# Optimization experiments

Measured on AMD Instinct MI355X. Metric: run time of the kernel, lower is better.

Reference implementation:

```python
import jax, jax.numpy as jnp
import numpy as np

B, CIN, H, W = 64, 1, 64, 64
L = 6            # layer_number -> 2^L = 64 blocks per axis
T = 4            # chebyshev_number
C4 = 4 * T * T   # per-block channel width = 64
WK = H // 2 ** (L - 1)  # first-layer kernel/stride = 2
LEFT = H // 2 ** L      # leftover_x = leftover_y = 1


def setup_inputs() -> dict:
    key = jax.random.key(0)
    ks = jax.random.split(key, 16)
    d = {}
    d["x_real"] = jax.random.normal(ks[0], (B, CIN, H, W), jnp.float32)
    d["x_imag"] = jax.random.normal(ks[1], (B, CIN, H, W), jnp.float32)
    # layer 0: per-input-channel conv, 4 -> 4*C4 channels, kernel=stride=WK
    d["w0"] = jax.random.normal(ks[2], (CIN, 4 * C4, 4, WK, WK), jnp.float32) / float(np.sqrt(4 * WK * WK))
    d["b0"] = jnp.zeros((CIN, 4 * C4), jnp.float32)
    # recursion layers lyr=1..L-1: one conv per (channel, block), C4 -> 4*C4, kernel 2x2 stride 2
    for lyr in range(1, L):
        G = 2 ** lyr
        d["w%d" % lyr] = jax.random.normal(ks[2 + lyr], (CIN, G, G, 4 * C4, C4, 2, 2), jnp.float32) / float(np.sqrt(4 * C4))
        d["b%d" % lyr] = jnp.zeros((CIN, G, G, 4 * C4), jnp.float32)
    # final layer: 1x1 conv per block, C4 -> 4*LEFT*LEFT
    GL = 2 ** L
    d["wf"] = jax.random.normal(ks[10], (CIN, GL, GL, 4 * LEFT * LEFT, C4), jnp.float32) / float(np.sqrt(C4))
    d["bf"] = jnp.zeros((CIN, GL, GL, 4 * LEFT * LEFT), jnp.float32)
    return d


def _forward(x_real, x_imag, w0, b0, wrec, brec, wf, bf):
    # split(): [relu(re), relu(im), relu(-re), relu(-im)] per input channel
    xs = jax.nn.relu(jnp.stack([x_real, x_imag, -x_real, -x_imag], axis=2))  # (B,CIN,4,H,W)
    # layer 0: kernel=stride=WK conv as blocked einsum -> (B,CIN,4*C4,P,P), P = 2^(L-1)
    P = H // WK
    xb = xs.reshape(B, CIN, 4, P, WK, P, WK)
    y = jnp.einsum('bcipkql,coikl->bcopq', xb, w0) + b0[None, :, :, None, None]
    y = jax.nn.relu(y)
    # output channels = 2x2 block grid x C4; layout (B,CIN,gy,gx,C4,S,S)
    G, S = 2, P
    y = y.reshape(B, CIN, G, G, C4, S, S)
    for lyr in range(1, L):
        w, b = wrec[lyr - 1], brec[lyr - 1]
        S2 = S // 2
        # 2x2/stride-2 conv per block as batched einsum
        yb = y.reshape(B, CIN, G, G, C4, S2, 2, S2, 2)
        z = jnp.einsum('bcghipkql,cghoikl->bcghopq', yb, w) + b[None, :, :, :, :, None, None]
        z = jax.nn.relu(z)
        # out channels split into (y_loc,x_loc,C4); child block = (2*gy+y_loc, 2*gx+x_loc)
        z = z.reshape(B, CIN, G, G, 2, 2, C4, S2, S2)
        z = z.transpose(0, 1, 2, 4, 3, 5, 6, 7, 8).reshape(B, CIN, 2 * G, 2 * G, C4, S2, S2)
        y, G, S = z, 2 * G, S2
    # final layer: spatial S == 1, 1x1 conv per block
    yv = y[..., 0, 0]                                     # (B,CIN,GL,GL,C4)
    f = jnp.einsum('bcghi,cghoi->bcgho', yv, wf) + bf[None]
    f = jax.nn.relu(f)
    # out channel o = 4*(ky*LEFT+kx)+comp; pixel = (gy*LEFT+ky, gx*LEFT+kx)
    f = f.reshape(B, CIN, G, G, LEFT, LEFT, 4)
    f = f.transpose(0, 1, 2, 4, 3, 5, 6).reshape(B, CIN, H, W, 4)
    # joint(): real = comp0 - comp2, then scale by 1/(H*W)
    return (f[..., 0] - f[..., 2]) / (H * W)


def reference(x_real, x_imag, w0, b0, w1, b1, w2, b2, w3, b3, w4, b4, w5, b5, wf, bf):
    return _forward(x_real, x_imag, w0, b0, (w1, w2, w3, w4, w5), (b1, b2, b3, b4, b5), wf, bf)
```

## Files before the change

kernel.cpp:

```cpp
#include <hip/hip_runtime.h>
#include <cstddef>


typedef unsigned int  u32;
typedef unsigned short u16;
typedef __attribute__((ext_vector_type(8))) short bf16x8;
typedef __attribute__((ext_vector_type(4))) float f32x4;

#define PLANE 16777216

__device__ inline u16 bf16_rn(float x) {
    u32 u = __builtin_bit_cast(u32, x);
    u32 r = (u + 0x7FFFu + ((u >> 16) & 1u)) >> 16;
    return (u16)r;
}
__device__ inline float bf16_to_f(u16 h) {
    u32 u = ((u32)h) << 16;
    return __builtin_bit_cast(float, u);
}
__device__ inline u32 pack_split(float v) {
    const u16 h = bf16_rn(v);
    const u16 l = bf16_rn(v - bf16_to_f(h));
    return (u32)h | ((u32)l << 16);
}
__device__ inline void bar_lds() {
    asm volatile("s_waitcnt lgkmcnt(0)\n\ts_barrier" ::: "memory");
}

__global__ __launch_bounds__(256)
void wconv_kernel(const float* __restrict__ src, u16* __restrict__ hi,
                  u16* __restrict__ lo, int n8) {
    const int i = blockIdx.x * 256 + threadIdx.x;
    if (i >= n8) return;
    const float4 a = *(const float4*)(src + 8 * i);
    const float4 b = *(const float4*)(src + 8 * i + 4);
    union { bf16x8 v; u16 u[8]; } H, L;
    const float f[8] = {a.x, a.y, a.z, a.w, b.x, b.y, b.z, b.w};
#pragma unroll
    for (int e = 0; e < 8; ++e) {
        const u16 h = bf16_rn(f[e]);
        H.u[e] = h;
        L.u[e] = bf16_rn(f[e] - bf16_to_f(h));
    }
    *(bf16x8*)(hi + 8 * i) = H.v;
    *(bf16x8*)(lo + 8 * i) = L.v;
}

__global__ __launch_bounds__(256)
void layer0_kernel(const float* __restrict__ xr, const float* __restrict__ xi,
                   const float* __restrict__ w0, const float* __restrict__ b0,
                   u32* __restrict__ A1) {
    __shared__ float w0s[128][16];
    __shared__ float b0s[128];
    const int og  = blockIdx.y;
    const int tid = threadIdx.x;
    {
        const int row = tid >> 1, half = tid & 1;
        const float4 wa = *(const float4*)(w0 + (og * 128 + row) * 16 + half * 8);
        const float4 wb = *(const float4*)(w0 + (og * 128 + row) * 16 + half * 8 + 4);
        *(float4*)&w0s[row][half * 8]     = wa;
        *(float4*)&w0s[row][half * 8 + 4] = wb;
        if (tid < 128) b0s[tid] = b0[og * 128 + tid];
    }
    __syncthreads();

    const int n = blockIdx.x * 256 + tid;
    const int b = n >> 10, p = (n >> 5) & 31, q = n & 31;
    float xs[16];
#pragma unroll
    for (int k = 0; k < 2; ++k) {
        const float2 vr = *(const float2*)(xr + b * 4096 + (2 * p + k) * 64 + 2 * q);
        const float2 vi = *(const float2*)(xi + b * 4096 + (2 * p + k) * 64 + 2 * q);
        xs[0  + k * 2 + 0] = fmaxf(vr.x, 0.f);  xs[0  + k * 2 + 1] = fmaxf(vr.y, 0.f);
        xs[4  + k * 2 + 0] = fmaxf(vi.x, 0.f);  xs[4  + k * 2 + 1] = fmaxf(vi.y, 0.f);
        xs[8  + k * 2 + 0] = fmaxf(-vr.x, 0.f); xs[8  + k * 2 + 1] = fmaxf(-vr.y, 0.f);
        xs[12 + k * 2 + 0] = fmaxf(-vi.x, 0.f); xs[12 + k * 2 + 1] = fmaxf(-vi.y, 0.f);
    }
    const int kp = p & 1, lp = q & 1, pp = p >> 1, qp = q >> 1;
    const size_t pixoff = (size_t)(b * 256 + pp * 16 + qp);
#pragma unroll
    for (int j = 0; j < 128; ++j) {
        float acc = b0s[j];
#pragma unroll
        for (int e = 0; e < 16; ++e) acc = fmaf(xs[e], w0s[j][e], acc);
        acc = fmaxf(acc, 0.f);
        const int o = og * 128 + j;
        const int gy = o >> 7, gx = (o >> 6) & 1, c = o & 63;
        const size_t flat = (size_t)((((gy * 2 + gx) * 64 + c) * 2 + kp) * 2 + lp) * (64 * 256)
                          + pixoff;
        A1[flat] = pack_split(acc);
    }
}

template<int NT, bool PRECONV>
__global__ __launch_bounds__(256, 2)
void rec_mfma_kernel(const u32* __restrict__ Yg,
                     const float* __restrict__ Wf,
                     const u16* __restrict__ Whi_g, const u16* __restrict__ Wlo_g,
                     const float* __restrict__ bias, u32* __restrict__ Aout,
                     const int lgG, const int lgS2) {
    constexpr int NF  = NT / 16;
    constexpr int LD  = 40;
    constexpr int NCP = NT / 2;
    constexpr int NRG = 256 / NCP;
    constexpr int RPT = 32 / NRG;

    __shared__ u16 Yhi_s[NT * LD];
    __shared__ u16 Ylo_s[NT * LD];

    const int G  = 1 << lgG;
    const int S2 = 1 << lgS2;
    const int Nb = 64 << (2 * lgS2);

    int bid, nt;
    const int nBid = G * G, NTILES = gridDim.x;
    if (nBid >= 8) {
        const int h = blockIdx.z * NTILES + blockIdx.x;
        const int xcd = h & 7, j = h >> 3, per = nBid >> 3;
        bid = xcd * per + j / NTILES;
        nt  = j % NTILES;
    } else { bid = blockIdx.z; nt = blockIdx.x; }

    const size_t wbase = (size_t)bid * 65536;
    const u32* Yblk = Yg + (size_t)bid * 256 * (size_t)Nb + (size_t)nt * NT;

    const int tid = threadIdx.x, wave = tid >> 6, lane = tid & 63;
    const int l16 = lane & 15, lk = lane >> 4;
    const int cp = tid % NCP, rg = tid / NCP;
    const int col0 = cp * 2, trow = rg * RPT;

    f32x4 acc[4][NF];
#pragma unroll
    for (int m = 0; m < 4; ++m)
#pragma unroll
        for (int n = 0; n < NF; ++n)
            acc[m][n] = (f32x4){0.f, 0.f, 0.f, 0.f};

    uint2  yreg[2][RPT];
    float4 wv[2][8];
    bf16x8 wh[4], wl[4];
    u32 yhw[2][RPT / 2], ylw[2][RPT / 2];

    auto loadY = [&](int ybuf, int k0) {
#pragma unroll
        for (int r = 0; r < RPT; ++r)
            yreg[ybuf][r] = *(const uint2*)(Yblk + (size_t)(k0 + trow + r) * Nb + col0);
    };
    auto loadWpre = [&](int k0) {
#pragma unroll
        for (int m = 0; m < 4; ++m) {
            const size_t off = wbase + (size_t)(wave * 64 + m * 16 + l16) * 256 + k0 + lk * 8;
            wh[m] = *(const bf16x8*)(Whi_g + off);
            wl[m] = *(const bf16x8*)(Wlo_g + off);
        }
    };
    auto loadWf32 = [&](int wbuf, int k0) {
#pragma unroll
        for (int m = 0; m < 4; ++m) {
            const float* wr = Wf + wbase + (size_t)(wave * 64 + m * 16 + l16) * 256 + k0 + lk * 8;
            wv[wbuf][2 * m]     = *(const float4*)wr;
            wv[wbuf][2 * m + 1] = *(const float4*)(wr + 4);
        }
    };
    auto convW = [&](int wbuf) {
#pragma unroll
        for (int m = 0; m < 4; ++m) {
            const float f[8] = { wv[wbuf][2 * m].x,     wv[wbuf][2 * m].y,
                                 wv[wbuf][2 * m].z,     wv[wbuf][2 * m].w,
                                 wv[wbuf][2 * m + 1].x, wv[wbuf][2 * m + 1].y,
                                 wv[wbuf][2 * m + 1].z, wv[wbuf][2 * m + 1].w };
            union { bf16x8 v; u16 u[8]; } H, L;
#pragma unroll
            for (int e = 0; e < 8; ++e) {
                const u16 hh = bf16_rn(f[e]);
                H.u[e] = hh;
                L.u[e] = bf16_rn(f[e] - bf16_to_f(hh));
            }
            wh[m] = H.v;
            wl[m] = L.v;
        }
    };
    auto prepY = [&](int ybuf) {
#pragma unroll
        for (int c = 0; c < 2; ++c)
#pragma unroll
            for (int j2 = 0; j2 < RPT / 2; ++j2) {
                const u32 a = c ? yreg[ybuf][2 * j2].y     : yreg[ybuf][2 * j2].x;
                const u32 b = c ? yreg[ybuf][2 * j2 + 1].y : yreg[ybuf][2 * j2 + 1].x;
                yhw[c][j2] = (a & 0xFFFFu) | (b << 16);
                ylw[c][j2] = (a >> 16)     | (b & 0xFFFF0000u);
            }
    };
    auto stageY = [&]() {
#pragma unroll
        for (int c = 0; c < 2; ++c) {
            if constexpr (RPT == 8) {
                *(uint4*)&Yhi_s[(col0 + c) * LD + trow] = make_uint4(yhw[c][0], yhw[c][1], yhw[c][2], yhw[c][3]);
                *(uint4*)&Ylo_s[(col0 + c) * LD + trow] = make_uint4(ylw[c][0], ylw[c][1], ylw[c][2], ylw[c][3]);
            } else {
                *(uint2*)&Yhi_s[(col0 + c) * LD + trow] = make_uint2(yhw[c][0], yhw[c][1]);
                *(uint2*)&Ylo_s[(col0 + c) * LD + trow] = make_uint2(ylw[c][0], ylw[c][1]);
            }
        }
    };

    if constexpr (PRECONV) { loadY(0, 0); loadY(1, 32); }
    else { loadWf32(0, 0); loadY(0, 0); loadWf32(1, 32); loadY(1, 32); }

#pragma unroll
    for (int it = 0; it < 8; ++it) {
        const int k0 = it * 32;
        const int cur = it & 1;
        if constexpr (PRECONV) loadWpre(k0);
        else convW(cur);
        prepY(cur);
        bar_lds();
        stageY();
        bar_lds();
        if constexpr (PRECONV) {
            if (it + 2 < 8) loadY(cur, k0 + 64);
        } else {
            if (it + 2 < 8) { loadWf32(cur, k0 + 64); loadY(cur, k0 + 64); }
        }
        __builtin_amdgcn_s_setprio(1);
#pragma unroll
        for (int n = 0; n < NF; ++n) {
            const int ccol = n * 16 + l16;
            const bf16x8 bhi = *(const bf16x8*)&Yhi_s[ccol * LD + 8 * lk];
            const bf16x8 blo = *(const bf16x8*)&Ylo_s[ccol * LD + 8 * lk];
#pragma unroll
            for (int m = 0; m < 4; ++m)
                acc[m][n] = __builtin_amdgcn_mfma_f32_16x16x32_bf16(wh[m], bhi, acc[m][n], 0, 0, 0);
#pragma unroll
            for (int m = 0; m < 4; ++m)
                acc[m][n] = __builtin_amdgcn_mfma_f32_16x16x32_bf16(wh[m], blo, acc[m][n], 0, 0, 0);
#pragma unroll
            for (int m = 0; m < 4; ++m)
                acc[m][n] = __builtin_amdgcn_mfma_f32_16x16x32_bf16(wl[m], bhi, acc[m][n], 0, 0, 0);
        }
        __builtin_amdgcn_s_setprio(0);
    }

    const int gy = bid >> lgG, gx = bid & (G - 1);
    const int NS2 = S2 >> 1;
#pragma unroll
    for (int m = 0; m < 4; ++m) {
#pragma unroll
        for (int r = 0; r < 4; ++r) {
            const int oc = wave * 64 + m * 16 + lk * 4 + r;
            const float bi = bias[(size_t)bid * 256 + oc];
            const int yl = oc >> 7, xl = (oc >> 6) & 1, cch = oc & 63;
            const int cy = 2 * gy + yl, cx = 2 * gx + xl;
            const size_t base = (size_t)((cy * (2 * G) + cx) * 64 + cch);
#pragma unroll
            for (int n = 0; n < NF; ++n) {
                const float v = fmaxf(acc[m][n][r] + bi, 0.f);
                const int ng = nt * NT + n * 16 + l16;
                const int b   = ng >> (2 * lgS2);
                const int rem = ng & ((1 << (2 * lgS2)) - 1);
                const int p = rem >> lgS2, q = rem & (S2 - 1);
                const size_t flat = ((base * 2 + (p & 1)) * 2 + (q & 1)) * (size_t)(64 * NS2 * NS2)
                                  + (size_t)(b * NS2 * NS2 + (p >> 1) * NS2 + (q >> 1));
                Aout[flat] = pack_split(v);
            }
        }
    }
}

__global__ __launch_bounds__(256, 2)
void rec5_final_kernel(const u32* __restrict__ Yg, const float* __restrict__ Wf,
                       const float* __restrict__ bias, const float* __restrict__ wf,
                       const float* __restrict__ bff, float* __restrict__ out) {
    constexpr int NF = 4, LD = 40, RPT = 4;

    __shared__ u16 Yhi_s[64 * LD];
    __shared__ u16 Ylo_s[64 * LD];

    const int bid = blockIdx.x;
    const size_t wbase = (size_t)bid * 65536;
    const u32* Yblk = Yg + (size_t)bid * 256 * 64;

    const int tid = threadIdx.x, wave = tid >> 6, lane = tid & 63;
    const int l16 = lane & 15, lk = lane >> 4;
    const int cp = tid & 31, rg = tid >> 5;
    const int col0 = cp * 2, trow = rg * RPT;

    f32x4 acc[4][NF];
#pragma unroll
    for (int m = 0; m < 4; ++m)
#pragma unroll
        for (int n = 0; n < NF; ++n)
            acc[m][n] = (f32x4){0.f, 0.f, 0.f, 0.f};

    uint2  yreg[2][RPT];
    float4 wv[2][8];
    bf16x8 wh[4], wl[4];
    u32 yhw[2][RPT / 2], ylw[2][RPT / 2];

    auto loadY = [&](int ybuf, int k0) {
#pragma unroll
        for (int r = 0; r < RPT; ++r)
            yreg[ybuf][r] = *(const uint2*)(Yblk + (size_t)(k0 + trow + r) * 64 + col0);
    };
    auto loadWf32 = [&](int wbuf, int k0) {
#pragma unroll
        for (int m = 0; m < 4; ++m) {
            const float* wr = Wf + wbase + (size_t)(wave * 64 + m * 16 + l16) * 256 + k0 + lk * 8;
            wv[wbuf][2 * m]     = *(const float4*)wr;
            wv[wbuf][2 * m + 1] = *(const float4*)(wr + 4);
        }
    };
    auto convW = [&](int wbuf) {
#pragma unroll
        for (int m = 0; m < 4; ++m) {
            const float f[8] = { wv[wbuf][2 * m].x,     wv[wbuf][2 * m].y,
                                 wv[wbuf][2 * m].z,     wv[wbuf][2 * m].w,
                                 wv[wbuf][2 * m + 1].x, wv[wbuf][2 * m + 1].y,
                                 wv[wbuf][2 * m + 1].z, wv[wbuf][2 * m + 1].w };
            union { bf16x8 v; u16 u[8]; } H, L;
#pragma unroll
            for (int e = 0; e < 8; ++e) {
                const u16 hh = bf16_rn(f[e]);
                H.u[e] = hh;
                L.u[e] = bf16_rn(f[e] - bf16_to_f(hh));
            }
            wh[m] = H.v;
            wl[m] = L.v;
        }
    };

    loadWf32(0, 0); loadY(0, 0); loadWf32(1, 32); loadY(1, 32);

#pragma unroll
    for (int it = 0; it < 8; ++it) {
        const int k0 = it * 32;
        const int cur = it & 1;
        convW(cur);
#pragma unroll
        for (int c = 0; c < 2; ++c)
#pragma unroll
            for (int j2 = 0; j2 < RPT / 2; ++j2) {
                const u32 a = c ? yreg[cur][2 * j2].y     : yreg[cur][2 * j2].x;
                const u32 b = c ? yreg[cur][2 * j2 + 1].y : yreg[cur][2 * j2 + 1].x;
                yhw[c][j2] = (a & 0xFFFFu) | (b << 16);
                ylw[c][j2] = (a >> 16)     | (b & 0xFFFF0000u);
            }
        bar_lds();
#pragma unroll
        for (int c = 0; c < 2; ++c) {
            *(uint2*)&Yhi_s[(col0 + c) * LD + trow] = make_uint2(yhw[c][0], yhw[c][1]);
            *(uint2*)&Ylo_s[(col0 + c) * LD + trow] = make_uint2(ylw[c][0], ylw[c][1]);
        }
        bar_lds();
        if (it + 2 < 8) { loadWf32(cur, k0 + 64); loadY(cur, k0 + 64); }
        __builtin_amdgcn_s_setprio(1);
#pragma unroll
        for (int n = 0; n < NF; ++n) {
            const int ccol = n * 16 + l16;
            const bf16x8 bhi = *(const bf16x8*)&Yhi_s[ccol * LD + 8 * lk];
            const bf16x8 blo = *(const bf16x8*)&Ylo_s[ccol * LD + 8 * lk];
#pragma unroll
            for (int m = 0; m < 4; ++m)
                acc[m][n] = __builtin_amdgcn_mfma_f32_16x16x32_bf16(wh[m], bhi, acc[m][n], 0, 0, 0);
#pragma unroll
            for (int m = 0; m < 4; ++m)
                acc[m][n] = __builtin_amdgcn_mfma_f32_16x16x32_bf16(wh[m], blo, acc[m][n], 0, 0, 0);
#pragma unroll
            for (int m = 0; m < 4; ++m)
                acc[m][n] = __builtin_amdgcn_mfma_f32_16x16x32_bf16(wl[m], bhi, acc[m][n], 0, 0, 0);
        }
        __builtin_amdgcn_s_setprio(0);
    }

    const int gy = bid >> 5, gx = bid & 31;
    const int cy = 2 * gy + (wave >> 1), cx = 2 * gx + (wave & 1);
    const int blk = cy * 64 + cx;
    float wf0v[4][4], wf2v[4][4], biv[4][4];
#pragma unroll
    for (int m = 0; m < 4; ++m)
#pragma unroll
        for (int r = 0; r < 4; ++r) {
            const int cch = m * 16 + lk * 4 + r;
            wf0v[m][r] = wf[(size_t)blk * 256 + cch];
            wf2v[m][r] = wf[(size_t)blk * 256 + 128 + cch];
            biv[m][r]  = bias[(size_t)bid * 256 + wave * 64 + cch];
        }
    const float bf0 = bff[blk * 4 + 0], bf2 = bff[blk * 4 + 2];
#pragma unroll
    for (int n = 0; n < 4; ++n) {
        float a0 = 0.f, a2 = 0.f;
#pragma unroll
        for (int m = 0; m < 4; ++m)
#pragma unroll
            for (int r = 0; r < 4; ++r) {
                const float y = fmaxf(acc[m][n][r] + biv[m][r], 0.f);
                a0 = fmaf(y, wf0v[m][r], a0);
                a2 = fmaf(y, wf2v[m][r], a2);
            }
        a0 += __shfl_xor(a0, 16); a0 += __shfl_xor(a0, 32);
        a2 += __shfl_xor(a2, 16); a2 += __shfl_xor(a2, 32);
        if (lk == n) {
            const float o0 = fmaxf(a0 + bf0, 0.f);
            const float o2 = fmaxf(a2 + bf2, 0.f);
            out[(size_t)(n * 16 + l16) * 4096 + blk] = (o0 - o2) * (1.0f / 4096.0f);
        }
    }
}

extern "C" void kernel_launch(void* const* d_in, const int* in_sizes, int n_in,
                              void* d_out, int out_size, void* d_ws, size_t ws_size,
                              hipStream_t stream) {
    (void)in_sizes; (void)n_in; (void)out_size; (void)ws_size;

    const float* xr = (const float*)d_in[0];
    const float* xi = (const float*)d_in[1];
    const float* w0 = (const float*)d_in[2];
    const float* b0 = (const float*)d_in[3];
    const float* wrec[5] = { (const float*)d_in[4],  (const float*)d_in[6],
                             (const float*)d_in[8],  (const float*)d_in[10],
                             (const float*)d_in[12] };
    const float* brec[5] = { (const float*)d_in[5],  (const float*)d_in[7],
                             (const float*)d_in[9],  (const float*)d_in[11],
                             (const float*)d_in[13] };
    const float* wf = (const float*)d_in[14];
    const float* bf = (const float*)d_in[15];
    float* out = (float*)d_out;

    u32* bufA = (u32*)d_ws;
    u32* bufB = bufA + (size_t)PLANE;
    u16* wc1  = (u16*)(bufB + (size_t)PLANE);
    u16* wc2  = wc1 + (size_t)2 * 262144;
    u16* wc3  = wc2 + (size_t)2 * 1048576;

    wconv_kernel<<<(262144 / 8 + 255) / 256, 256, 0, stream>>>(wrec[0], wc1, wc1 + 262144, 262144 / 8);
    wconv_kernel<<<(1048576 / 8 + 255) / 256, 256, 0, stream>>>(wrec[1], wc2, wc2 + 1048576, 1048576 / 8);
    wconv_kernel<<<(4194304 / 8 + 255) / 256, 256, 0, stream>>>(wrec[2], wc3, wc3 + 4194304, 4194304 / 8);

    layer0_kernel<<<dim3(256, 2), 256, 0, stream>>>(xr, xi, w0, b0, bufA);

    rec_mfma_kernel<128, true><<<dim3(128, 1, 4), 256, 0, stream>>>(
        bufA, nullptr, wc1, wc1 + 262144, brec[0], bufB, 1, 4);
    rec_mfma_kernel<128, true><<<dim3(32, 1, 16), 256, 0, stream>>>(
        bufB, nullptr, wc2, wc2 + 1048576, brec[1], bufA, 2, 3);
    rec_mfma_kernel<128, true><<<dim3(8, 1, 64), 256, 0, stream>>>(
        bufA, nullptr, wc3, wc3 + 4194304, brec[2], bufB, 3, 2);
    rec_mfma_kernel<64, false><<<dim3(4, 1, 256), 256, 0, stream>>>(
        bufB, wrec[3], nullptr, nullptr, brec[3], bufA, 4, 1);
    rec5_final_kernel<<<1024, 256, 0, stream>>>(bufA, wrec[4], brec[4], wf, bf, out);
}
```

Measured before the change: 320.1 us.

## Fuse recursion layers 4 and 5 with final layer; merge weight conversion launches

Layer 4's conv is fused into the layer-5+final kernel. Each block computes one child's 64 output channels of layer 4 directly from the parent activations using register-held B fragments. It then stages the ReLU'd split-bf16 result in LDS as the B operand for layer 5. This removes the intermediate global write/read of layer-4 activations and one kernel launch, but the parent input and weight slice are read by 4 blocks. The three weight-conversion launches are merged into one kernel with range-based dispatch.

```diff
diff --git a/kernel.cpp b/kernel.cpp
--- a/kernel.cpp
+++ b/kernel.cpp
@@ -28,12 +28,16 @@
 }
 
 __global__ __launch_bounds__(256)
-void wconv_kernel(const float* __restrict__ src, u16* __restrict__ hi,
-                  u16* __restrict__ lo, int n8) {
+void wconv_all_kernel(const float* __restrict__ s1, const float* __restrict__ s2,
+                      const float* __restrict__ s3,
+                      u16* __restrict__ d1, u16* __restrict__ d2, u16* __restrict__ d3) {
     const int i = blockIdx.x * 256 + threadIdx.x;
-    if (i >= n8) return;
-    const float4 a = *(const float4*)(src + 8 * i);
-    const float4 b = *(const float4*)(src + 8 * i + 4);
+    const float* s; u16 *dh, *dl; int off;
+    if (i < 32768)        { s = s1; dh = d1; dl = d1 + 262144;  off = i; }
+    else if (i < 163840)  { s = s2; dh = d2; dl = d2 + 1048576; off = i - 32768; }
+    else                  { s = s3; dh = d3; dl = d3 + 4194304; off = i - 163840; }
+    const float4 a = *(const float4*)(s + 8 * off);
+    const float4 b = *(const float4*)(s + 8 * off + 4);
     union { bf16x8 v; u16 u[8]; } H, L;
     const float f[8] = {a.x, a.y, a.z, a.w, b.x, b.y, b.z, b.w};
 #pragma unroll
@@ -42,8 +46,8 @@
         H.u[e] = h;
         L.u[e] = bf16_rn(f[e] - bf16_to_f(h));
     }
-    *(bf16x8*)(hi + 8 * i) = H.v;
-    *(bf16x8*)(lo + 8 * i) = L.v;
+    *(bf16x8*)(dh + 8 * off) = H.v;
+    *(bf16x8*)(dl + 8 * off) = L.v;
 }
 
 __global__ __launch_bounds__(256)
@@ -92,18 +96,16 @@
     }
 }
 
-template<int NT, bool PRECONV>
+template<int NT>
 __global__ __launch_bounds__(256, 2)
 void rec_mfma_kernel(const u32* __restrict__ Yg,
-                     const float* __restrict__ Wf,
                      const u16* __restrict__ Whi_g, const u16* __restrict__ Wlo_g,
                      const float* __restrict__ bias, u32* __restrict__ Aout,
                      const int lgG, const int lgS2) {
     constexpr int NF  = NT / 16;
     constexpr int LD  = 40;
     constexpr int NCP = NT / 2;
-    constexpr int NRG = 256 / NCP;
-    constexpr int RPT = 32 / NRG;
+    constexpr int RPT = 32 / (256 / NCP);
 
     __shared__ u16 Yhi_s[NT * LD];
     __shared__ u16 Ylo_s[NT * LD];
@@ -137,7 +139,6 @@
             acc[m][n] = (f32x4){0.f, 0.f, 0.f, 0.f};
 
     uint2  yreg[2][RPT];
-    float4 wv[2][8];
     bf16x8 wh[4], wl[4];
     u32 yhw[2][RPT / 2], ylw[2][RPT / 2];
 
@@ -152,32 +153,6 @@
             const size_t off = wbase + (size_t)(wave * 64 + m * 16 + l16) * 256 + k0 + lk * 8;
             wh[m] = *(const bf16x8*)(Whi_g + off);
             wl[m] = *(const bf16x8*)(Wlo_g + off);
-        }
-    };
-    auto loadWf32 = [&](int wbuf, int k0) {
-#pragma unroll
-        for (int m = 0; m < 4; ++m) {
-            const float* wr = Wf + wbase + (size_t)(wave * 64 + m * 16 + l16) * 256 + k0 + lk * 8;
-            wv[wbuf][2 * m]     = *(const float4*)wr;
-            wv[wbuf][2 * m + 1] = *(const float4*)(wr + 4);
-        }
-    };
-    auto convW = [&](int wbuf) {
-#pragma unroll
-        for (int m = 0; m < 4; ++m) {
-            const float f[8] = { wv[wbuf][2 * m].x,     wv[wbuf][2 * m].y,
-                                 wv[wbuf][2 * m].z,     wv[wbuf][2 * m].w,
-                                 wv[wbuf][2 * m + 1].x, wv[wbuf][2 * m + 1].y,
-                                 wv[wbuf][2 * m + 1].z, wv[wbuf][2 * m + 1].w };
-            union { bf16x8 v; u16 u[8]; } H, L;
-#pragma unroll
-            for (int e = 0; e < 8; ++e) {
-                const u16 hh = bf16_rn(f[e]);
-                H.u[e] = hh;
-                L.u[e] = bf16_rn(f[e] - bf16_to_f(hh));
-            }
-            wh[m] = H.v;
-            wl[m] = L.v;
         }
     };
     auto prepY = [&](int ybuf) {
@@ -204,24 +179,18 @@
         }
     };
 
-    if constexpr (PRECONV) { loadY(0, 0); loadY(1, 32); }
-    else { loadWf32(0, 0); loadY(0, 0); loadWf32(1, 32); loadY(1, 32); }
+    loadY(0, 0); loadY(1, 32);
 
 #pragma unroll
     for (int it = 0; it < 8; ++it) {
         const int k0 = it * 32;
         const int cur = it & 1;
-        if constexpr (PRECONV) loadWpre(k0);
-        else convW(cur);
+        loadWpre(k0);
         prepY(cur);
         bar_lds();
         stageY();
         bar_lds();
-        if constexpr (PRECONV) {
-            if (it + 2 < 8) loadY(cur, k0 + 64);
-        } else {
-            if (it + 2 < 8) { loadWf32(cur, k0 + 64); loadY(cur, k0 + 64); }
-        }
+        if (it + 2 < 8) loadY(cur, k0 + 64);
         __builtin_amdgcn_s_setprio(1);
 #pragma unroll
         for (int n = 0; n < NF; ++n) {
@@ -268,55 +237,70 @@
 }
 
 __global__ __launch_bounds__(256, 2)
-void rec5_final_kernel(const u32* __restrict__ Yg, const float* __restrict__ Wf,
-                       const float* __restrict__ bias, const float* __restrict__ wf,
-                       const float* __restrict__ bff, float* __restrict__ out) {
-    constexpr int NF = 4, LD = 40, RPT = 4;
-
-    __shared__ u16 Yhi_s[64 * LD];
-    __shared__ u16 Ylo_s[64 * LD];
-
-    const int bid = blockIdx.x;
-    const size_t wbase = (size_t)bid * 65536;
-    const u32* Yblk = Yg + (size_t)bid * 256 * 64;
+void rec45_final_kernel(const u32* __restrict__ Yg, const float* __restrict__ W4,
+                        const float* __restrict__ b4, const float* __restrict__ W5,
+                        const float* __restrict__ b5, const float* __restrict__ wf,
+                        const float* __restrict__ bff, float* __restrict__ out) {
+    constexpr int LDW = 72;
+    __shared__ u16 Whi_w[64 * LDW];
+    __shared__ u16 Wlo_w[64 * LDW];
+
+    const int h = blockIdx.x;
+    const int parent = ((h >> 5) << 3) | (h & 7);
+    const int child  = (h >> 3) & 3;
+    const int pgy = parent >> 4, pgx = parent & 15;
+    const int cy = 2 * pgy + (child >> 1), cx = 2 * pgx + (child & 1);
+    const int bid5 = cy * 32 + cx;
+    const int ocbase = child * 64;
+
+    const u32* Yblk  = Yg + (size_t)parent * 65536;
+    const float* W4s = W4 + (size_t)parent * 65536 + (size_t)ocbase * 256;
+    const float* W5b = W5 + (size_t)bid5 * 65536;
 
     const int tid = threadIdx.x, wave = tid >> 6, lane = tid & 63;
     const int l16 = lane & 15, lk = lane >> 4;
-    const int cp = tid & 31, rg = tid >> 5;
-    const int col0 = cp * 2, trow = rg * RPT;
-
-    f32x4 acc[4][NF];
+
+    f32x4 acc1[4][4];
 #pragma unroll
     for (int m = 0; m < 4; ++m)
 #pragma unroll
-        for (int n = 0; n < NF; ++n)
-            acc[m][n] = (f32x4){0.f, 0.f, 0.f, 0.f};
-
-    uint2  yreg[2][RPT];
+        for (int n = 0; n < 4; ++n)
+            acc1[m][n] = (f32x4){0.f, 0.f, 0.f, 0.f};
+
+    u32    yf[2][4][8];
     float4 wv[2][8];
     bf16x8 wh[4], wl[4];
-    u32 yhw[2][RPT / 2], ylw[2][RPT / 2];
-
-    auto loadY = [&](int ybuf, int k0) {
-#pragma unroll
-        for (int r = 0; r < RPT; ++r)
-            yreg[ybuf][r] = *(const uint2*)(Yblk + (size_t)(k0 + trow + r) * 64 + col0);
-    };
-    auto loadWf32 = [&](int wbuf, int k0) {
+
+    auto loadY = [&](int buf, int k0) {
+#pragma unroll
+        for (int n = 0; n < 4; ++n)
+#pragma unroll
+            for (int j = 0; j < 8; ++j)
+                yf[buf][n][j] = Yblk[(size_t)(k0 + 8 * lk + j) * 256 + wave * 64 + n * 16 + l16];
+    };
+    auto loadW4 = [&](int buf, int k0) {
 #pragma unroll
         for (int m = 0; m < 4; ++m) {
-            const float* wr = Wf + wbase + (size_t)(wave * 64 + m * 16 + l16) * 256 + k0 + lk * 8;
-            wv[wbuf][2 * m]     = *(const float4*)wr;
-            wv[wbuf][2 * m + 1] = *(const float4*)(wr + 4);
-        }
-    };
-    auto convW = [&](int wbuf) {
+            const float* p = W4s + (size_t)(m * 16 + l16) * 256 + k0 + lk * 8;
+            wv[buf][2 * m]     = *(const float4*)p;
+            wv[buf][2 * m + 1] = *(const float4*)(p + 4);
+        }
+    };
+    auto loadW5 = [&](int buf, int t) {
 #pragma unroll
         for (int m = 0; m < 4; ++m) {
-            const float f[8] = { wv[wbuf][2 * m].x,     wv[wbuf][2 * m].y,
-                                 wv[wbuf][2 * m].z,     wv[wbuf][2 * m].w,
-                                 wv[wbuf][2 * m + 1].x, wv[wbuf][2 * m + 1].y,
-                                 wv[wbuf][2 * m + 1].z, wv[wbuf][2 * m + 1].w };
+            const float* p = W5b + (size_t)(wave * 64 + m * 16 + l16) * 256 + t * 32 + lk * 8;
+            wv[buf][2 * m]     = *(const float4*)p;
+            wv[buf][2 * m + 1] = *(const float4*)(p + 4);
+        }
+    };
+    auto convW = [&](int buf) {
+#pragma unroll
+        for (int m = 0; m < 4; ++m) {
+            const float f[8] = { wv[buf][2 * m].x,     wv[buf][2 * m].y,
+                                 wv[buf][2 * m].z,     wv[buf][2 * m].w,
+                                 wv[buf][2 * m + 1].x, wv[buf][2 * m + 1].y,
+                                 wv[buf][2 * m + 1].z, wv[buf][2 * m + 1].w };
             union { bf16x8 v; u16 u[8]; } H, L;
 #pragma unroll
             for (int e = 0; e < 8; ++e) {
@@ -329,52 +313,96 @@
         }
     };
 
-    loadWf32(0, 0); loadY(0, 0); loadWf32(1, 32); loadY(1, 32);
-
+    loadY(0, 0); loadW4(0, 0); loadY(1, 32); loadW4(1, 32);
 #pragma unroll
     for (int it = 0; it < 8; ++it) {
-        const int k0 = it * 32;
         const int cur = it & 1;
         convW(cur);
-#pragma unroll
-        for (int c = 0; c < 2; ++c)
-#pragma unroll
-            for (int j2 = 0; j2 < RPT / 2; ++j2) {
-                const u32 a = c ? yreg[cur][2 * j2].y     : yreg[cur][2 * j2].x;
-                const u32 b = c ? yreg[cur][2 * j2 + 1].y : yreg[cur][2 * j2 + 1].x;
-                yhw[c][j2] = (a & 0xFFFFu) | (b << 16);
-                ylw[c][j2] = (a >> 16)     | (b & 0xFFFF0000u);
-            }
+        __builtin_amdgcn_s_setprio(1);
+#pragma unroll
+        for (int n = 0; n < 4; ++n) {
+            union { bf16x8 v; u16 u[8]; } BH, BL;
+#pragma unroll
+            for (int j = 0; j < 8; ++j) {
+                const u32 y = yf[cur][n][j];
+                BH.u[j] = (u16)y;
+                BL.u[j] = (u16)(y >> 16);
+            }
+#pragma unroll
+            for (int m = 0; m < 4; ++m)
+                acc1[m][n] = __builtin_amdgcn_mfma_f32_16x16x32_bf16(wh[m], BH.v, acc1[m][n], 0, 0, 0);
+#pragma unroll
+            for (int m = 0; m < 4; ++m)
+                acc1[m][n] = __builtin_amdgcn_mfma_f32_16x16x32_bf16(wh[m], BL.v, acc1[m][n], 0, 0, 0);
+#pragma unroll
+            for (int m = 0; m < 4; ++m)
+                acc1[m][n] = __builtin_amdgcn_mfma_f32_16x16x32_bf16(wl[m], BH.v, acc1[m][n], 0, 0, 0);
+        }
+        __builtin_amdgcn_s_setprio(0);
+        if (it + 2 < 8) { loadY(cur, 32 * it + 64); loadW4(cur, 32 * it + 64); }
+    }
+
+    f32x4 acc2[4][4];
+#pragma unroll
+    for (int m = 0; m < 4; ++m)
+#pragma unroll
+        for (int n = 0; n < 4; ++n)
+            acc2[m][n] = (f32x4){0.f, 0.f, 0.f, 0.f};
+
+    float b4v[4][4];
+#pragma unroll
+    for (int kw = 0; kw < 4; ++kw)
+#pragma unroll
+        for (int r = 0; r < 4; ++r)
+            b4v[kw][r] = b4[(size_t)parent * 256 + ocbase + kw * 16 + lk * 4 + r];
+
+    loadW5(0, 0); loadW5(1, 1);
+
+#pragma unroll
+    for (int kw = 0; kw < 4; ++kw) {
+#pragma unroll
+        for (int n = 0; n < 4; ++n) {
+            const int colg = wave * 64 + n * 16 + l16;
+            const int b_ = colg >> 2, par = colg & 3;
+#pragma unroll
+            for (int r = 0; r < 4; ++r) {
+                const float v = fmaxf(acc1[kw][n][r] + b4v[kw][r], 0.f);
+                const int k_ = lk * 16 + r * 4 + par;
+                const u16 hh = bf16_rn(v);
+                Whi_w[b_ * LDW + k_] = hh;
+                Wlo_w[b_ * LDW + k_] = bf16_rn(v - bf16_to_f(hh));
+            }
+        }
         bar_lds();
 #pragma unroll
-        for (int c = 0; c < 2; ++c) {
-            *(uint2*)&Yhi_s[(col0 + c) * LD + trow] = make_uint2(yhw[c][0], yhw[c][1]);
-            *(uint2*)&Ylo_s[(col0 + c) * LD + trow] = make_uint2(ylw[c][0], ylw[c][1]);
+        for (int kc = 0; kc < 2; ++kc) {
+            const int t = kw * 2 + kc;
+            const int cur = t & 1;
+            convW(cur);
+            __builtin_amdgcn_s_setprio(1);
+#pragma unroll
+            for (int n = 0; n < 4; ++n) {
+                const int b_ = n * 16 + l16;
+                const bf16x8 bhi = *(const bf16x8*)&Whi_w[b_ * LDW + kc * 32 + 8 * lk];
+                const bf16x8 blo = *(const bf16x8*)&Wlo_w[b_ * LDW + kc * 32 + 8 * lk];
+#pragma unroll
+                for (int m = 0; m < 4; ++m)
+                    acc2[m][n] = __builtin_amdgcn_mfma_f32_16x16x32_bf16(wh[m], bhi, acc2[m][n], 0, 0, 0);
+#pragma unroll
+                for (int m = 0; m < 4; ++m)
+                    acc2[m][n] = __builtin_amdgcn_mfma_f32_16x16x32_bf16(wh[m], blo, acc2[m][n], 0, 0, 0);
+#pragma unroll
+                for (int m = 0; m < 4; ++m)
+                    acc2[m][n] = __builtin_amdgcn_mfma_f32_16x16x32_bf16(wl[m], bhi, acc2[m][n], 0, 0, 0);
+            }
+            __builtin_amdgcn_s_setprio(0);
+            if (t + 2 < 8) loadW5(cur, t + 2);
         }
         bar_lds();
-        if (it + 2 < 8) { loadWf32(cur, k0 + 64); loadY(cur, k0 + 64); }
-        __builtin_amdgcn_s_setprio(1);
-#pragma unroll
-        for (int n = 0; n < NF; ++n) {
-            const int ccol = n * 16 + l16;
-            const bf16x8 bhi = *(const bf16x8*)&Yhi_s[ccol * LD + 8 * lk];
-            const bf16x8 blo = *(const bf16x8*)&Ylo_s[ccol * LD + 8 * lk];
-#pragma unroll
-            for (int m = 0; m < 4; ++m)
-                acc[m][n] = __builtin_amdgcn_mfma_f32_16x16x32_bf16(wh[m], bhi, acc[m][n], 0, 0, 0);
-#pragma unroll
-            for (int m = 0; m < 4; ++m)
-                acc[m][n] = __builtin_amdgcn_mfma_f32_16x16x32_bf16(wh[m], blo, acc[m][n], 0, 0, 0);
-#pragma unroll
-            for (int m = 0; m < 4; ++m)
-                acc[m][n] = __builtin_amdgcn_mfma_f32_16x16x32_bf16(wl[m], bhi, acc[m][n], 0, 0, 0);
-        }
-        __builtin_amdgcn_s_setprio(0);
-    }
-
-    const int gy = bid >> 5, gx = bid & 31;
-    const int cy = 2 * gy + (wave >> 1), cx = 2 * gx + (wave & 1);
-    const int blk = cy * 64 + cx;
+    }
+
+    const int fy = 2 * cy + (wave >> 1), fx = 2 * cx + (wave & 1);
+    const int blk = fy * 64 + fx;
     float wf0v[4][4], wf2v[4][4], biv[4][4];
 #pragma unroll
     for (int m = 0; m < 4; ++m)
@@ -383,7 +411,7 @@
             const int cch = m * 16 + lk * 4 + r;
             wf0v[m][r] = wf[(size_t)blk * 256 + cch];
             wf2v[m][r] = wf[(size_t)blk * 256 + 128 + cch];
-            biv[m][r]  = bias[(size_t)bid * 256 + wave * 64 + cch];
+            biv[m][r]  = b5[(size_t)bid5 * 256 + wave * 64 + cch];
         }
     const float bf0 = bff[blk * 4 + 0], bf2 = bff[blk * 4 + 2];
 #pragma unroll
@@ -393,7 +421,7 @@
         for (int m = 0; m < 4; ++m)
 #pragma unroll
             for (int r = 0; r < 4; ++r) {
-                const float y = fmaxf(acc[m][n][r] + biv[m][r], 0.f);
+                const float y = fmaxf(acc2[m][n][r] + biv[m][r], 0.f);
                 a0 = fmaf(y, wf0v[m][r], a0);
                 a2 = fmaf(y, wf2v[m][r], a2);
             }
@@ -432,19 +460,16 @@
     u16* wc2  = wc1 + (size_t)2 * 262144;
     u16* wc3  = wc2 + (size_t)2 * 1048576;
 
-    wconv_kernel<<<(262144 / 8 + 255) / 256, 256, 0, stream>>>(wrec[0], wc1, wc1 + 262144, 262144 / 8);
-    wconv_kernel<<<(1048576 / 8 + 255) / 256, 256, 0, stream>>>(wrec[1], wc2, wc2 + 1048576, 1048576 / 8);
-    wconv_kernel<<<(4194304 / 8 + 255) / 256, 256, 0, stream>>>(wrec[2], wc3, wc3 + 4194304, 4194304 / 8);
+    wconv_all_kernel<<<2688, 256, 0, stream>>>(wrec[0], wrec[1], wrec[2], wc1, wc2, wc3);
 
     layer0_kernel<<<dim3(256, 2), 256, 0, stream>>>(xr, xi, w0, b0, bufA);
 
-    rec_mfma_kernel<128, true><<<dim3(128, 1, 4), 256, 0, stream>>>(
-        bufA, nullptr, wc1, wc1 + 262144, brec[0], bufB, 1, 4);
-    rec_mfma_kernel<128, true><<<dim3(32, 1, 16), 256, 0, stream>>>(
-        bufB, nullptr, wc2, wc2 + 1048576, brec[1], bufA, 2, 3);
-    rec_mfma_kernel<128, true><<<dim3(8, 1, 64), 256, 0, stream>>>(
-        bufA, nullptr, wc3, wc3 + 4194304, brec[2], bufB, 3, 2);
-    rec_mfma_kernel<64, false><<<dim3(4, 1, 256), 256, 0, stream>>>(
-        bufB, wrec[3], nullptr, nullptr, brec[3], bufA, 4, 1);
-    rec5_final_kernel<<<1024, 256, 0, stream>>>(bufA, wrec[4], brec[4], wf, bf, out);
-}
+    rec_mfma_kernel<128><<<dim3(128, 1, 4), 256, 0, stream>>>(
+        bufA, wc1, wc1 + 262144, brec[0], bufB, 1, 4);
+    rec_mfma_kernel<128><<<dim3(32, 1, 16), 256, 0, stream>>>(
+        bufB, wc2, wc2 + 1048576, brec[1], bufA, 2, 3);
+    rec_mfma_kernel<128><<<dim3(8, 1, 64), 256, 0, stream>>>(
+        bufA, wc3, wc3 + 4194304, brec[2], bufB, 3, 2);
+    rec45_final_kernel<<<1024, 256, 0, stream>>>(
+        bufB, wrec[3], brec[3], wrec[4], brec[4], wf, bf, out);
+}
```

After: 270.6 us. 15.5% less time.
